# Kernel tuning notes

Hardware: AMD Instinct MI355X
Metric: run time of the kernel (lower is better)

The kernel has to match this reference:

```python
import jax, jax.numpy as jnp
import numpy as np

N = 10000        # nodes
E = 320000       # edges (avg degree 32)
NF_IN = 256
NF_OUT = 512
EPS = 1e-5


def batch_norm(x, gamma, beta):
    # BatchNorm1d training-mode: biased stats over the node (batch) dim
    mu = jnp.mean(x, axis=0)
    var = jnp.var(x, axis=0)
    return (x - mu) * jax.lax.rsqrt(var + EPS) * gamma + beta


def sage_conv(x, src, dst, W_l, W_r, bias):
    # PyG SAGEConv, aggr='mean': out = lin_l(mean_{j->i} x_j) + lin_r(x_i)
    msg = x[src]                                             # [E, F]
    s = jax.ops.segment_sum(msg, dst, num_segments=N)        # [N, F]
    cnt = jax.ops.segment_sum(jnp.ones((msg.shape[0], 1), x.dtype), dst, num_segments=N)
    mean = s / jnp.maximum(cnt, 1.0)
    return mean @ W_l + bias + x @ W_r


def setup_inputs() -> dict:
    key = jax.random.key(0)
    ks = jax.random.split(key, 8)
    x = jax.random.normal(ks[0], (N, NF_IN), jnp.float32)
    edge_index = jax.random.randint(ks[1], (2, E), 0, N, dtype=jnp.int64)
    s_in = 0.02
    return {
        "x": x,
        "edge_index": edge_index,
        "gamma0": jnp.ones((NF_IN,), jnp.float32),
        "beta0": jnp.zeros((NF_IN,), jnp.float32),
        "W0_l": jax.random.normal(ks[2], (NF_IN, NF_OUT), jnp.float32) * s_in,
        "W0_r": jax.random.normal(ks[3], (NF_IN, NF_OUT), jnp.float32) * s_in,
        "bias0": jnp.zeros((NF_OUT,), jnp.float32),
        "gamma1": jnp.ones((NF_OUT,), jnp.float32),
        "beta1": jnp.zeros((NF_OUT,), jnp.float32),
        "W1_l": jax.random.normal(ks[4], (NF_OUT, NF_OUT), jnp.float32) * s_in,
        "W1_r": jax.random.normal(ks[5], (NF_OUT, NF_OUT), jnp.float32) * s_in,
        "bias1": jnp.zeros((NF_OUT,), jnp.float32),
        "W_sc": jax.random.normal(ks[6], (NF_IN, NF_OUT), jnp.float32) * s_in,
        "b_sc": jnp.zeros((NF_OUT,), jnp.float32),
    }


def reference(x, edge_index, gamma0, beta0, W0_l, W0_r, bias0,
              gamma1, beta1, W1_l, W1_r, bias1, W_sc, b_sc):
    src, dst = edge_index[0], edge_index[1]
    h = jax.nn.relu(batch_norm(x, gamma0, beta0))
    h = sage_conv(h, src, dst, W0_l, W0_r, bias0)
    h = jax.nn.relu(batch_norm(h, gamma1, beta1))
    h = sage_conv(h, src, dst, W1_l, W1_r, bias1)
    x_sc = x @ W_sc + b_sc  # nin_shortcut since nf_in != nf_out
    return x_sc + h
```

## Files before the change

### kernel.cpp

```cpp
#include <hip/hip_runtime.h>
#include <hip/hip_bf16.h>
#include <cstdint>
#include <cstddef>

#define N_NODES 10000
#define N_EDGES 320000
#define FIN 256
#define FOUT 512
#define BN_EPS 1e-5f
#define DEG_CAP 96
#define SLICE_CAP 18
#define NRANGES 20
#define NSLICES 16
#define NODES_PER_RANGE (N_NODES / NRANGES)
#define EDGES_PER_SLICE (N_EDGES / NSLICES)
#define SCAN_BLOCKS (NRANGES * NSLICES)

typedef unsigned short ushort_t;
typedef unsigned char uchar_t;
typedef __attribute__((ext_vector_type(8))) short short8;
typedef __attribute__((ext_vector_type(4))) float f32x4;
typedef __attribute__((ext_vector_type(2))) float f32x2;
typedef __attribute__((ext_vector_type(4))) unsigned short ushort4v;
typedef __attribute__((ext_vector_type(8))) unsigned short ushort8v;

__device__ inline ushort_t f2bf(float f) {
  __hip_bfloat16 h = __float2bfloat16(f);
  return *reinterpret_cast<ushort_t*>(&h);
}
__device__ inline float bf2f(ushort_t u) {
  union { unsigned int i; float f; } c;
  c.i = ((unsigned int)u) << 16;
  return c.f;
}
__device__ inline uchar_t f2q(float v) {
  return (uchar_t)(__builtin_amdgcn_cvt_pk_fp8_f32(v, v, 0u, false) & 0xffu);
}
__device__ inline void q4_to_f32(unsigned int w, float* o) {
  f32x2 lo = __builtin_amdgcn_cvt_pk_f32_fp8(w, false);
  f32x2 hi = __builtin_amdgcn_cvt_pk_f32_fp8(w, true);
  o[0] = lo[0]; o[1] = lo[1]; o[2] = hi[0]; o[3] = hi[1];
}

__global__ void zero_k(int* __restrict__ p, int n) {
  int i = blockIdx.x * blockDim.x + threadIdx.x;
  if (i < n) p[i] = 0;
}

__global__ __launch_bounds__(256)
void prologue_k(const int* __restrict__ src, const int* __restrict__ dst,
                int* __restrict__ fill, int* __restrict__ csrc,
                const float* __restrict__ W0l, const float* __restrict__ W0r,
                const float* __restrict__ Wsc, const float* __restrict__ W1l,
                const float* __restrict__ W1r, const float* __restrict__ bias1,
                const float* __restrict__ bsc,
                ushort_t* __restrict__ w0lt, ushort_t* __restrict__ w0rt,
                ushort_t* __restrict__ wsct, ushort_t* __restrict__ w1lt,
                ushort_t* __restrict__ w1rt, float* __restrict__ cbias,
                const float* __restrict__ x, float* __restrict__ sums0,
                ushort_t* __restrict__ xb, uchar_t* __restrict__ xq) {
  __shared__ __align__(16) char smem[512 * 4 + NODES_PER_RANGE * SLICE_CAP * 4];
  int b = blockIdx.x;
  int tid = threadIdx.x;

  if (b < SCAN_BLOCKS) {
    int range = b / NSLICES;
    int slice = b % NSLICES;
    int lo = range * NODES_PER_RANGE;
    int* lcnt = (int*)smem;
    int* lbuf = lcnt + 512;
    for (int i = tid; i < NODES_PER_RANGE; i += 256) lcnt[i] = 0;
    __syncthreads();

    int e0 = slice * EDGES_PER_SLICE;
    const int4* dst4 = (const int4*)(dst + e0);
    const int4* src4 = (const int4*)(src + e0);
    const int nvec = EDGES_PER_SLICE / 4;
    for (int v = tid; v < nvec; v += 256) {
      int4 d4 = dst4[v];
      int4 s4 = src4[v];
      int dd[4] = {d4.x, d4.y, d4.z, d4.w};
      int ss[4] = {s4.x, s4.y, s4.z, s4.w};
#pragma unroll
      for (int j = 0; j < 4; ++j) {
        int d = dd[j] - lo;
        if (d >= 0 && d < NODES_PER_RANGE) {
          int pos = atomicAdd(&lcnt[d], 1);
          if (pos < SLICE_CAP) lbuf[d * SLICE_CAP + pos] = ss[j];
        }
      }
    }
    __syncthreads();

    for (int i = tid; i < NODES_PER_RANGE; i += 256) {
      int cnt = min(lcnt[i], SLICE_CAP);
      if (cnt > 0) {
        int off = atomicAdd(&fill[lo + i], cnt);
        int wmax = min(cnt, DEG_CAP - off);
        for (int k = 0; k < wmax; ++k)
          csrc[(size_t)(lo + i) * DEG_CAP + off + k] = lbuf[i * SLICE_CAP + k];
      }
    }
    return;
  }

  if (b < SCAN_BLOCKS + 897) {
    int bb = b - SCAN_BLOCKS;
    if (bb == 896) {
      cbias[tid] = bias1[tid] + bsc[tid];
      cbias[tid + 256] = bias1[tid + 256] + bsc[tid + 256];
      return;
    }
    const float* W;
    ushort_t* Wt;
    int K, t;
    if (bb < 384) {
      K = 256; t = bb & 127;
      if (bb < 128)      { W = W0l; Wt = w0lt; }
      else if (bb < 256) { W = W0r; Wt = w0rt; }
      else               { W = Wsc; Wt = wsct; }
    } else {
      K = 512; t = (bb - 384) & 255;
      if (bb < 640) { W = W1l; Wt = w1lt; }
      else          { W = W1r; Wt = w1rt; }
    }
    ushort_t (*tl)[40] = (ushort_t(*)[40])smem;
    int Kt = K >> 5;
    int bk = (t % Kt) * 32, bn = (t / Kt) * 32;
    int tx = tid & 31, ty = tid >> 5;
#pragma unroll
    for (int i = 0; i < 4; ++i)
      tl[ty + i * 8][tx] = f2bf(W[(size_t)(bk + ty + i * 8) * 512 + bn + tx]);
    __syncthreads();
#pragma unroll
    for (int i = 0; i < 4; ++i)
      Wt[(size_t)(bn + ty + i * 8) * K + bk + tx] = tl[tx][ty + i * 8];
    return;
  }

  int blk = b - (SCAN_BLOCKS + 897);
  int c = tid;
  int r0 = blk * 80, r1 = r0 + 80;
  float s = 0.f, q = 0.f;
  for (int r = r0; r < r1; ++r) {
    float v = x[(size_t)r * FIN + c];
    s += v;
    q = fmaf(v, v, q);
    xb[(size_t)r * FIN + c] = f2bf(v);
    xq[(size_t)r * FIN + c] = f2q(v);
  }
  atomicAdd(&sums0[c], s);
  atomicAdd(&sums0[FIN + c], q);
}

template <int F>
__global__ __launch_bounds__(64)
void gather_mean_q8(const uchar_t* __restrict__ H, const int* __restrict__ fill,
                    const int* __restrict__ csrc, const float* __restrict__ sums,
                    const float* __restrict__ gamma, const float* __restrict__ beta,
                    float invN, ushort_t* __restrict__ agg) {
  constexpr int VEC = F / 64;
  int node = blockIdx.x;
  int c0 = threadIdx.x * VEC;
  float sc[VEC], sh[VEC];
#pragma unroll
  for (int j = 0; j < VEC; ++j) {
    float mu = sums[c0 + j] * invN;
    float var = fmaf(-mu, mu, sums[F + c0 + j] * invN);
    float s = rsqrtf(var + BN_EPS) * gamma[c0 + j];
    sc[j] = s;
    sh[j] = fmaf(-mu, s, beta[c0 + j]);
  }
  int deg = fill[node];
  int lim = min(deg, DEG_CAP);
  const int* cs = csrc + (size_t)node * DEG_CAP;
  float acc[VEC] = {};
  int e = 0;
  for (; e + 2 <= lim; e += 2) {
    int s0 = cs[e], s1 = cs[e + 1];
    float va[VEC], vb[VEC];
    if constexpr (VEC == 8) {
      uint2 ua = *(const uint2*)&H[(size_t)s0 * F + c0];
      uint2 ub = *(const uint2*)&H[(size_t)s1 * F + c0];
      q4_to_f32(ua.x, va); q4_to_f32(ua.y, va + 4);
      q4_to_f32(ub.x, vb); q4_to_f32(ub.y, vb + 4);
    } else {
      unsigned int ua = *(const unsigned int*)&H[(size_t)s0 * F + c0];
      unsigned int ub = *(const unsigned int*)&H[(size_t)s1 * F + c0];
      q4_to_f32(ua, va);
      q4_to_f32(ub, vb);
    }
#pragma unroll
    for (int j = 0; j < VEC; ++j)
      acc[j] += fmaxf(fmaf(va[j], sc[j], sh[j]), 0.f) +
                fmaxf(fmaf(vb[j], sc[j], sh[j]), 0.f);
  }
  if (e < lim) {
    int s0 = cs[e];
    float va[VEC];
    if constexpr (VEC == 8) {
      uint2 ua = *(const uint2*)&H[(size_t)s0 * F + c0];
      q4_to_f32(ua.x, va); q4_to_f32(ua.y, va + 4);
    } else {
      unsigned int ua = *(const unsigned int*)&H[(size_t)s0 * F + c0];
      q4_to_f32(ua, va);
    }
#pragma unroll
    for (int j = 0; j < VEC; ++j) acc[j] += fmaxf(fmaf(va[j], sc[j], sh[j]), 0.f);
  }
  float ic = 1.0f / fmaxf((float)deg, 1.0f);
  if constexpr (VEC == 8) {
    ushort8v o;
#pragma unroll
    for (int j = 0; j < 8; ++j) o[j] = f2bf(acc[j] * ic);
    *(ushort8v*)&agg[(size_t)node * F + c0] = o;
  } else {
    ushort4v o;
#pragma unroll
    for (int j = 0; j < 4; ++j) o[j] = f2bf(acc[j] * ic);
    *(ushort4v*)&agg[(size_t)node * F + c0] = o;
  }
}

template <int EPI, int K0, int K1, int K2, bool STATS, int BNS, int KBN, bool WQ>
__global__ __launch_bounds__(256)
void gemm_mfma(const ushort_t* __restrict__ A0, const ushort_t* __restrict__ B0,
               const ushort_t* __restrict__ A1p, const ushort_t* __restrict__ B1p,
               const ushort_t* __restrict__ A2p, const ushort_t* __restrict__ B2p,
               const float* __restrict__ bias, void* __restrict__ Cv,
               uchar_t* __restrict__ Cq, int M,
               const float* __restrict__ sums, const float* __restrict__ gamma,
               const float* __restrict__ beta, float invN,
               float* __restrict__ statsOut) {
  __shared__ __align__(16) short As[64][72];
  __shared__ __align__(16) short Bs[128][72];
  __shared__ float ab_s[2 * KBN];

  int tid = threadIdx.x;
  int lane = tid & 63;
  int w = tid >> 6;
  int wm = w >> 1, wn = w & 1;
  int m0 = blockIdx.y * 64;
  int n0 = blockIdx.x * 128;

  if constexpr (BNS >= 0) {
    for (int c = tid; c < KBN; c += 256) {
      float mu = sums[c] * invN;
      float var = fmaf(-mu, mu, sums[KBN + c] * invN);
      float s = rsqrtf(var + BN_EPS) * gamma[c];
      ab_s[c] = s;
      ab_s[KBN + c] = fmaf(-mu, s, beta[c]);
    }
    __syncthreads();
  }

  int ar = tid >> 2;
  int aq = (tid & 3) * 16;
  int br = tid >> 1;
  int bh = (tid & 1) * 32;
  bool arow_ok = (m0 + ar) < M;

  constexpr int NS = (K0 + K1 + K2) / 64;
  f32x4 acc[2][4] = {};

  short8 ra0, ra1, rb0, rb1, rb2, rb3;
  bool dobn_cur = false;
  int aboff_cur = 0;

  auto LOADSTEP = [&](int ks) {
    int k0 = ks * 64;
    const ushort_t* Ap;
    const ushort_t* Bp;
    int lk, KA;
    if (k0 < K0) { Ap = A0; Bp = B0; lk = k0; KA = K0; dobn_cur = (BNS == 0); }
    else if (k0 < K0 + K1) { Ap = A1p; Bp = B1p; lk = k0 - K0; KA = K1; dobn_cur = (BNS == 1); }
    else { Ap = A2p; Bp = B2p; lk = k0 - K0 - K1; KA = K2; dobn_cur = (BNS == 2); }
    aboff_cur = lk;
    if (arow_ok) {
      const short8* ap = (const short8*)&Ap[(size_t)(m0 + ar) * KA + lk + aq];
      ra0 = ap[0]; ra1 = ap[1];
    } else {
      ra0 = short8{}; ra1 = short8{};
    }
    const short8* bp = (const short8*)&Bp[(size_t)(n0 + br) * KA + lk + bh];
    rb0 = bp[0]; rb1 = bp[1]; rb2 = bp[2]; rb3 = bp[3];
  };

  LOADSTEP(0);
  for (int ks = 0; ks < NS; ++ks) {
    if constexpr (BNS >= 0) {
      if (dobn_cur && arow_ok) {
        const float* abp = &ab_s[aboff_cur + aq];
#pragma unroll
        for (int j = 0; j < 8; ++j) {
          ra0[j] = (short)f2bf(fmaxf(fmaf(bf2f((ushort_t)ra0[j]), abp[j], abp[KBN + j]), 0.f));
          ra1[j] = (short)f2bf(fmaxf(fmaf(bf2f((ushort_t)ra1[j]), abp[8 + j], abp[KBN + 8 + j]), 0.f));
        }
      }
    }
    *(short8*)&As[ar][aq] = ra0;
    *(short8*)&As[ar][aq + 8] = ra1;
    *(short8*)&Bs[br][bh] = rb0;
    *(short8*)&Bs[br][bh + 8] = rb1;
    *(short8*)&Bs[br][bh + 16] = rb2;
    *(short8*)&Bs[br][bh + 24] = rb3;
    __syncthreads();

    if (ks + 1 < NS) LOADSTEP(ks + 1);

#pragma unroll
    for (int ks2 = 0; ks2 < 2; ++ks2) {
      int kof = ks2 * 32 + (lane >> 4) * 8;
      int rsel = lane & 15;
      short8 af[2], bfv[4];
      af[0] = *(const short8*)&As[wm * 32 + rsel][kof];
      af[1] = *(const short8*)&As[wm * 32 + 16 + rsel][kof];
#pragma unroll
      for (int ni = 0; ni < 4; ++ni)
        bfv[ni] = *(const short8*)&Bs[wn * 64 + ni * 16 + rsel][kof];
#pragma unroll
      for (int mi = 0; mi < 2; ++mi)
#pragma unroll
        for (int ni = 0; ni < 4; ++ni)
          acc[mi][ni] = __builtin_amdgcn_mfma_f32_16x16x32_bf16(
              af[mi], bfv[ni], acc[mi][ni], 0, 0, 0);
    }
    __syncthreads();
  }

  float* st = (float*)&As[0][0];
  if constexpr (STATS) {
    if (tid < 256) st[tid] = 0.f;
    __syncthreads();
  }

  int colbase = n0 + wn * 64 + (lane & 15);
  int rowq = (lane >> 4) * 4;
#pragma unroll
  for (int ni = 0; ni < 4; ++ni) {
    int col = colbase + ni * 16;
    float bv = bias[col];
    float s_l = 0.f, q_l = 0.f;
#pragma unroll
    for (int mi = 0; mi < 2; ++mi) {
      int rbase = m0 + wm * 32 + mi * 16 + rowq;
#pragma unroll
      for (int r = 0; r < 4; ++r) {
        int row = rbase + r;
        if (row < M) {
          float v = acc[mi][ni][r] + bv;
          if constexpr (STATS) {
            s_l += v;
            q_l = fmaf(v, v, q_l);
          }
          if constexpr (EPI == 0) {
            ((ushort_t*)Cv)[(size_t)row * 512 + col] = f2bf(v);
            if constexpr (WQ) Cq[(size_t)row * 512 + col] = f2q(v);
          } else {
            ((float*)Cv)[(size_t)row * 512 + col] = v;
          }
        }
      }
    }
    if constexpr (STATS) {
      int cloc = wn * 64 + ni * 16 + (lane & 15);
      atomicAdd(&st[cloc], s_l);
      atomicAdd(&st[128 + cloc], q_l);
    }
  }
  if constexpr (STATS) {
    __syncthreads();
    if (tid < 256) {
      int c = tid & 127;
      atomicAdd(&statsOut[(tid >> 7) * 512 + n0 + c], st[(tid >> 7) * 128 + c]);
    }
  }
}

extern "C" void kernel_launch(void* const* d_in, const int* in_sizes, int n_in,
                              void* d_out, int out_size, void* d_ws, size_t ws_size,
                              hipStream_t stream) {
  const float* x = (const float*)d_in[0];
  const int* ei = (const int*)d_in[1];
  const int* src = ei;
  const int* dst = ei + N_EDGES;
  const float* gamma0 = (const float*)d_in[2];
  const float* beta0  = (const float*)d_in[3];
  const float* W0l    = (const float*)d_in[4];
  const float* W0r    = (const float*)d_in[5];
  const float* bias0  = (const float*)d_in[6];
  const float* gamma1 = (const float*)d_in[7];
  const float* beta1  = (const float*)d_in[8];
  const float* W1l    = (const float*)d_in[9];
  const float* W1r    = (const float*)d_in[10];
  const float* bias1  = (const float*)d_in[11];
  const float* Wsc    = (const float*)d_in[12];
  const float* bsc    = (const float*)d_in[13];
  float* out = (float*)d_out;

  char* wp = (char*)d_ws;
  ushort_t* agg0b = (ushort_t*)wp; wp += (size_t)N_NODES * FIN * 2;
  ushort_t* h1b   = (ushort_t*)wp; wp += (size_t)N_NODES * FOUT * 2;
  ushort_t* agg1b = (ushort_t*)wp; wp += (size_t)N_NODES * FOUT * 2;
  ushort_t* xb    = (ushort_t*)wp; wp += (size_t)N_NODES * FIN * 2;
  uchar_t*  xq    = (uchar_t*)wp;  wp += (size_t)N_NODES * FIN;
  uchar_t*  h1q   = (uchar_t*)wp;  wp += (size_t)N_NODES * FOUT;
  ushort_t* w0lt  = (ushort_t*)wp; wp += (size_t)FIN * FOUT * 2;
  ushort_t* w0rt  = (ushort_t*)wp; wp += (size_t)FIN * FOUT * 2;
  ushort_t* wsct  = (ushort_t*)wp; wp += (size_t)FIN * FOUT * 2;
  ushort_t* w1lt  = (ushort_t*)wp; wp += (size_t)FOUT * FOUT * 2;
  ushort_t* w1rt  = (ushort_t*)wp; wp += (size_t)FOUT * FOUT * 2;
  float* cbias = (float*)wp; wp += FOUT * 4;
  float* sums0 = (float*)wp; wp += 2 * FIN * 4;
  float* sums1 = (float*)wp; wp += 2 * FOUT * 4;
  int* fill    = (int*)wp; wp += (size_t)N_NODES * 4;
  int* csrc    = (int*)wp; wp += (size_t)N_NODES * DEG_CAP * 4;

  const float invN = 1.0f / N_NODES;

  const int zwords = 2 * FIN + 2 * FOUT + N_NODES;
  zero_k<<<(zwords + 255) / 256, 256, 0, stream>>>((int*)sums0, zwords);

  prologue_k<<<SCAN_BLOCKS + 897 + 125, 256, 0, stream>>>(
      src, dst, fill, csrc, W0l, W0r, Wsc, W1l, W1r, bias1, bsc,
      w0lt, w0rt, wsct, w1lt, w1rt, cbias, x, sums0, xb, xq);

  gather_mean_q8<FIN><<<N_NODES, 64, 0, stream>>>(
      xq, fill, csrc, sums0, gamma0, beta0, invN, agg0b);

  gemm_mfma<0, FIN, FIN, 0, true, 1, FIN, true>
      <<<dim3(FOUT / 128, (N_NODES + 63) / 64), 256, 0, stream>>>(
      agg0b, w0lt, xb, w0rt, nullptr, nullptr, bias0, h1b, h1q, N_NODES,
      sums0, gamma0, beta0, invN, sums1);

  gather_mean_q8<FOUT><<<N_NODES, 64, 0, stream>>>(
      h1q, fill, csrc, sums1, gamma1, beta1, invN, agg1b);

  gemm_mfma<1, FOUT, FOUT, FIN, false, 1, FOUT, false>
      <<<dim3(FOUT / 128, (N_NODES + 63) / 64), 256, 0, stream>>>(
      agg1b, w1lt, h1b, w1rt, xb, wsct, cbias, out, nullptr, N_NODES,
      sums1, gamma1, beta1, invN, nullptr);
}
```

Measured before the change: 129.3 us.

## Use 512-thread GEMM blocks with XCD-aware 1D tile swizzle

```diff
diff --git a/kernel.cpp b/kernel.cpp
--- a/kernel.cpp
+++ b/kernel.cpp
@@ -223,7 +223,7 @@
 }
 
 template <int EPI, int K0, int K1, int K2, bool STATS, int BNS, int KBN, bool WQ>
-__global__ __launch_bounds__(256)
+__global__ __launch_bounds__(512)
 void gemm_mfma(const ushort_t* __restrict__ A0, const ushort_t* __restrict__ B0,
                const ushort_t* __restrict__ A1p, const ushort_t* __restrict__ B1p,
                const ushort_t* __restrict__ A2p, const ushort_t* __restrict__ B2p,
@@ -236,15 +236,24 @@
   __shared__ __align__(16) short Bs[128][72];
   __shared__ float ab_s[2 * KBN];
 
+  int wgid = blockIdx.x;
+  int cxcd = wgid & 7;
+  int j = wgid >> 3;
+  int nt = j & 3;
+  int yhi = j >> 2;
+  int y = cxcd + yhi * 8;
+  int MT = (M + 63) >> 6;
+  if (y >= MT) return;
+  int m0 = y * 64;
+  int n0 = nt * 128;
+
   int tid = threadIdx.x;
   int lane = tid & 63;
   int w = tid >> 6;
-  int wm = w >> 1, wn = w & 1;
-  int m0 = blockIdx.y * 64;
-  int n0 = blockIdx.x * 128;
+  int wm = w >> 2, wn = w & 3;
 
   if constexpr (BNS >= 0) {
-    for (int c = tid; c < KBN; c += 256) {
+    for (int c = tid; c < KBN; c += 512) {
       float mu = sums[c] * invN;
       float var = fmaf(-mu, mu, sums[KBN + c] * invN);
       float s = rsqrtf(var + BN_EPS) * gamma[c];
@@ -254,16 +263,16 @@
     __syncthreads();
   }
 
-  int ar = tid >> 2;
-  int aq = (tid & 3) * 16;
-  int br = tid >> 1;
-  int bh = (tid & 1) * 32;
+  int ar = tid >> 3;
+  int aq8 = (tid & 7) * 8;
+  int br = tid >> 2;
+  int bq = (tid & 3) * 16;
   bool arow_ok = (m0 + ar) < M;
 
   constexpr int NS = (K0 + K1 + K2) / 64;
-  f32x4 acc[2][4] = {};
-
-  short8 ra0, ra1, rb0, rb1, rb2, rb3;
+  f32x4 acc[2][2] = {};
+
+  short8 ra0, rb0, rb1;
   bool dobn_cur = false;
   int aboff_cur = 0;
 
@@ -277,33 +286,27 @@
     else { Ap = A2p; Bp = B2p; lk = k0 - K0 - K1; KA = K2; dobn_cur = (BNS == 2); }
     aboff_cur = lk;
     if (arow_ok) {
-      const short8* ap = (const short8*)&Ap[(size_t)(m0 + ar) * KA + lk + aq];
-      ra0 = ap[0]; ra1 = ap[1];
+      ra0 = *(const short8*)&Ap[(size_t)(m0 + ar) * KA + lk + aq8];
     } else {
-      ra0 = short8{}; ra1 = short8{};
-    }
-    const short8* bp = (const short8*)&Bp[(size_t)(n0 + br) * KA + lk + bh];
-    rb0 = bp[0]; rb1 = bp[1]; rb2 = bp[2]; rb3 = bp[3];
+      ra0 = short8{};
+    }
+    const short8* bp = (const short8*)&Bp[(size_t)(n0 + br) * KA + lk + bq];
+    rb0 = bp[0]; rb1 = bp[1];
   };
 
   LOADSTEP(0);
   for (int ks = 0; ks < NS; ++ks) {
     if constexpr (BNS >= 0) {
       if (dobn_cur && arow_ok) {
-        const float* abp = &ab_s[aboff_cur + aq];
-#pragma unroll
-        for (int j = 0; j < 8; ++j) {
-          ra0[j] = (short)f2bf(fmaxf(fmaf(bf2f((ushort_t)ra0[j]), abp[j], abp[KBN + j]), 0.f));
-          ra1[j] = (short)f2bf(fmaxf(fmaf(bf2f((ushort_t)ra1[j]), abp[8 + j], abp[KBN + 8 + j]), 0.f));
-        }
+        const float* abp = &ab_s[aboff_cur + aq8];
+#pragma unroll
+        for (int jj = 0; jj < 8; ++jj)
+          ra0[jj] = (short)f2bf(fmaxf(fmaf(bf2f((ushort_t)ra0[jj]), abp[jj], abp[KBN + jj]), 0.f));
       }
     }
-    *(short8*)&As[ar][aq] = ra0;
-    *(short8*)&As[ar][aq + 8] = ra1;
-    *(short8*)&Bs[br][bh] = rb0;
-    *(short8*)&Bs[br][bh + 8] = rb1;
-    *(short8*)&Bs[br][bh + 16] = rb2;
-    *(short8*)&Bs[br][bh + 24] = rb3;
+    *(short8*)&As[ar][aq8] = ra0;
+    *(short8*)&Bs[br][bq] = rb0;
+    *(short8*)&Bs[br][bq + 8] = rb1;
     __syncthreads();
 
     if (ks + 1 < NS) LOADSTEP(ks + 1);
@@ -312,16 +315,15 @@
     for (int ks2 = 0; ks2 < 2; ++ks2) {
       int kof = ks2 * 32 + (lane >> 4) * 8;
       int rsel = lane & 15;
-      short8 af[2], bfv[4];
+      short8 af[2], bfv[2];
       af[0] = *(const short8*)&As[wm * 32 + rsel][kof];
       af[1] = *(const short8*)&As[wm * 32 + 16 + rsel][kof];
-#pragma unroll
-      for (int ni = 0; ni < 4; ++ni)
-        bfv[ni] = *(const short8*)&Bs[wn * 64 + ni * 16 + rsel][kof];
+      bfv[0] = *(const short8*)&Bs[wn * 32 + rsel][kof];
+      bfv[1] = *(const short8*)&Bs[wn * 32 + 16 + rsel][kof];
 #pragma unroll
       for (int mi = 0; mi < 2; ++mi)
 #pragma unroll
-        for (int ni = 0; ni < 4; ++ni)
+        for (int ni = 0; ni < 2; ++ni)
           acc[mi][ni] = __builtin_amdgcn_mfma_f32_16x16x32_bf16(
               af[mi], bfv[ni], acc[mi][ni], 0, 0, 0);
     }
@@ -334,10 +336,10 @@
     __syncthreads();
   }
 
-  int colbase = n0 + wn * 64 + (lane & 15);
+  int colbase = n0 + wn * 32 + (lane & 15);
   int rowq = (lane >> 4) * 4;
 #pragma unroll
-  for (int ni = 0; ni < 4; ++ni) {
+  for (int ni = 0; ni < 2; ++ni) {
     int col = colbase + ni * 16;
     float bv = bias[col];
     float s_l = 0.f, q_l = 0.f;
@@ -363,7 +365,7 @@
       }
     }
     if constexpr (STATS) {
-      int cloc = wn * 64 + ni * 16 + (lane & 15);
+      int cloc = wn * 32 + ni * 16 + (lane & 15);
       atomicAdd(&st[cloc], s_l);
       atomicAdd(&st[128 + cloc], q_l);
     }
@@ -428,8 +430,10 @@
   gather_mean_q8<FIN><<<N_NODES, 64, 0, stream>>>(
       xq, fill, csrc, sums0, gamma0, beta0, invN, agg0b);
 
+  const int GEMM_GRID = 8 * 4 * ((((N_NODES + 63) / 64) + 7) / 8);
+
   gemm_mfma<0, FIN, FIN, 0, true, 1, FIN, true>
-      <<<dim3(FOUT / 128, (N_NODES + 63) / 64), 256, 0, stream>>>(
+      <<<GEMM_GRID, 512, 0, stream>>>(
       agg0b, w0lt, xb, w0rt, nullptr, nullptr, bias0, h1b, h1q, N_NODES,
       sums0, gamma0, beta0, invN, sums1);
 
@@ -437,7 +441,7 @@
       h1q, fill, csrc, sums1, gamma1, beta1, invN, agg1b);
 
   gemm_mfma<1, FOUT, FOUT, FIN, false, 1, FOUT, false>
-      <<<dim3(FOUT / 128, (N_NODES + 63) / 64), 256, 0, stream>>>(
+      <<<GEMM_GRID, 512, 0, stream>>>(
       agg1b, w1lt, h1b, w1rt, xb, wsct, cbias, out, nullptr, N_NODES,
       sums1, gamma1, beta1, invN, nullptr);
 }
```

After: 126.0 us. -2.6%, faster.
